# Kernel optimization log

Hardware: AMD Instinct MI355X
Metric: run time of the kernel (lower is better)

Reference implementation:

```python
import jax, jax.numpy as jnp
import numpy as np

C = 256          # C_in == C_out
G = C // 4       # groups = C_in/4 -> 4 channels per group
K = 3
STRIDE = 1
PAD = 2
DIL = 2
EPS = 1e-5

@jax.custom_vjp
def binarize(x):
    # 1-bit sign binarization with straight-through estimator (STE)
    return jnp.sign(x)

def _bin_fwd(x):
    return jnp.sign(x), x

def _bin_bwd(x, g):
    # STE with hardtanh clip: pass grad where |x| <= 1
    return (g * (jnp.abs(x) <= 1.0).astype(g.dtype),)

binarize.defvjp(_bin_fwd, _bin_bwd)

def setup_inputs() -> dict:
    key = jax.random.key(0)
    k1, k2, k3, k4, k5, k6 = jax.random.split(key, 6)
    x = jax.random.normal(k1, (64, C, 32, 32), jnp.float32)
    # grouped conv weight: [C_out, C_in/groups, K, K] = [256, 4, 3, 3]
    weight = jax.random.normal(k2, (C, C // G, K, K), jnp.float32) * 0.1
    gamma = 1.0 + 0.1 * jax.random.normal(k3, (C,), jnp.float32)
    beta = 0.1 * jax.random.normal(k4, (C,), jnp.float32)
    running_mean = 0.1 * jax.random.normal(k5, (C,), jnp.float32)
    running_var = jax.random.uniform(k6, (C,), jnp.float32, 0.5, 1.5)
    return {"x": x, "weight": weight, "gamma": gamma, "beta": beta,
            "running_mean": running_mean, "running_var": running_var}

def reference(x, weight, gamma, beta, running_mean, running_var):
    # BatchNorm2d (inference form with running stats)
    inv = gamma * jax.lax.rsqrt(running_var + EPS)            # [C]
    h = x * inv[None, :, None, None] + (beta - running_mean * inv)[None, :, None, None]
    # binarize activations and weights (1w1a)
    a = binarize(h)
    w = binarize(weight)
    # grouped dilated conv, stride 1, pad 2, dilation 2 -> same HxW
    out = jax.lax.conv_general_dilated(
        a, w,
        window_strides=(STRIDE, STRIDE),
        padding=[(PAD, PAD), (PAD, PAD)],
        rhs_dilation=(DIL, DIL),
        dimension_numbers=("NCHW", "OIHW", "NCHW"),
        feature_group_count=G)
    # channel shuffle: [N,C,H,W] -> [N,g,C/g,H,W] -> [N,C/g,g,H,W] -> [N,C,H,W]
    N, Cc, H, W = out.shape
    out = out.reshape(N, G, Cc // G, H, W).transpose(0, 2, 1, 3, 4).reshape(N, Cc, H, W)
    # identity shortcut (stride == 1)
    return out + x
```

## Files before the change

### kernel.cpp

```cpp
#include <hip/hip_runtime.h>

#ifndef __has_builtin
#define __has_builtin(x) 0
#endif

#if __has_builtin(__builtin_amdgcn_sdot4)
#define DOT4(a, b, c) __builtin_amdgcn_sdot4((a), (b), (c), false)
#else
__device__ __forceinline__ int dot4_sw(int a, int b, int c) {
#pragma unroll
    for (int k = 0; k < 4; ++k)
        c += (int)(signed char)((a >> (8 * k)) & 0xff) *
             (int)(signed char)((b >> (8 * k)) & 0xff);
    return c;
}
#define DOT4(a, b, c) dot4_sw((a), (b), (c))
#endif

#if __has_builtin(__builtin_amdgcn_sched_barrier)
#define SCHED_FENCE() __builtin_amdgcn_sched_barrier(0)
#else
#define SCHED_FENCE() asm volatile("" ::: "memory")
#endif

typedef float vfloat4 __attribute__((ext_vector_type(4)));

constexpr int CH   = 256;
constexpr int NPIX = 1024;
constexpr float BN_EPS = 1e-5f;

__global__ __launch_bounds__(64)
void bconv(const float* __restrict__ x,
           const float* __restrict__ wgt,
           const float* __restrict__ gamma,
           const float* __restrict__ beta,
           const float* __restrict__ rmean,
           const float* __restrict__ rvar,
           float* __restrict__ out) {
    const int lane = threadIdx.x;
    const int bid = blockIdx.x;
    const int swz = (bid & 7) * 2048 + (bid >> 3);
    const int oct = swz & 3;
    const int g   = (swz >> 2) & 63;
    const int n   = swz >> 8;

    const int row  = oct * 8 + (lane >> 3);
    const int col0 = (lane & 7) * 4;
    const int pix0 = row * 32 + col0;
    const float* xn = x + n * CH * NPIX;
    float* on = out + n * CH * NPIX;

    vfloat4 xv[3][4];
#pragma unroll
    for (int kh = 0; kh < 3; ++kh) {
        const int rsc = min(max(row + 2 * kh - 2, 0), 31);
        const float* rp = xn + g * 4 * NPIX + rsc * 32 + col0;
#pragma unroll
        for (int ci = 0; ci < 4; ++ci)
            xv[kh][ci] = *(const vfloat4*)(rp + ci * NPIX);
    }
    vfloat4 sc[4];
#pragma unroll
    for (int c2 = 0; c2 < 4; ++c2)
        sc[c2] = *(const vfloat4*)(xn + (c2 * 64 + g) * NPIX + pix0);
    SCHED_FENCE();

    const int* wb = (const int*)(wgt + g * 144);
    int wq[4][9];
#pragma unroll
    for (int c2 = 0; c2 < 4; ++c2)
#pragma unroll
        for (int t = 0; t < 9; ++t) {
            int pk = 0;
#pragma unroll
            for (int ci = 0; ci < 4; ++ci) {
                const int b = wb[c2 * 36 + ci * 9 + t];
                const int s = ((b & 0x7fffffff) == 0) ? 0 : ((b < 0) ? -1 : 1);
                pk |= (s & 0xff) << (8 * ci);
            }
            wq[c2][t] = pk;
        }

    float inv[4], bias[4];
#pragma unroll
    for (int ci = 0; ci < 4; ++ci) {
        const int c = g * 4 + ci;
        float r  = __fdiv_rn(1.0f, __fsqrt_rn(__fadd_rn(rvar[c], BN_EPS)));
        inv[ci]  = __fmul_rn(gamma[c], r);
        bias[ci] = __fsub_rn(beta[c], __fmul_rn(rmean[c], inv[ci]));
    }

    int pkc[3][4];
#pragma unroll
    for (int kh = 0; kh < 3; ++kh) {
        const bool ok = (unsigned)(row + 2 * kh - 2) < 32u;
#pragma unroll
        for (int p = 0; p < 4; ++p) {
            int v = 0;
#pragma unroll
            for (int ci = 0; ci < 4; ++ci) {
                float h = __fadd_rn(__fmul_rn(xv[kh][ci][p], inv[ci]), bias[ci]);
                int s = (h > 0.f) ? 1 : ((h < 0.f) ? -1 : 0);
                v |= (s & 0xff) << (8 * ci);
            }
            pkc[kh][p] = ok ? v : 0;
        }
    }

    const bool le = (col0 == 0), re = (col0 == 28);
    int a[3][8];
#pragma unroll
    for (int kh = 0; kh < 3; ++kh) {
        int l2 = __shfl_up(pkc[kh][2], 1);
        int l3 = __shfl_up(pkc[kh][3], 1);
        int r0 = __shfl_down(pkc[kh][0], 1);
        int r1 = __shfl_down(pkc[kh][1], 1);
        a[kh][0] = le ? 0 : l2;
        a[kh][1] = le ? 0 : l3;
        a[kh][2] = pkc[kh][0]; a[kh][3] = pkc[kh][1];
        a[kh][4] = pkc[kh][2]; a[kh][5] = pkc[kh][3];
        a[kh][6] = re ? 0 : r0;
        a[kh][7] = re ? 0 : r1;
    }

#pragma unroll
    for (int c2 = 0; c2 < 4; ++c2) {
        vfloat4 o;
#pragma unroll
        for (int p = 0; p < 4; ++p) {
            int acc = 0;
#pragma unroll
            for (int kh = 0; kh < 3; ++kh)
#pragma unroll
                for (int kw = 0; kw < 3; ++kw)
                    acc = DOT4(a[kh][p + 2 * kw], wq[c2][kh * 3 + kw], acc);
            o[p] = __fadd_rn((float)acc, sc[c2][p]);
        }
        __builtin_nontemporal_store(o, (vfloat4*)(on + (c2 * 64 + g) * NPIX + pix0));
    }
}

extern "C" void kernel_launch(void* const* d_in, const int* in_sizes, int n_in,
                              void* d_out, int out_size, void* d_ws, size_t ws_size,
                              hipStream_t stream) {
    const float* x     = (const float*)d_in[0];
    const float* wgt   = (const float*)d_in[1];
    const float* gamma = (const float*)d_in[2];
    const float* beta  = (const float*)d_in[3];
    const float* rmean = (const float*)d_in[4];
    const float* rvar  = (const float*)d_in[5];
    float* out = (float*)d_out;

    const int N = in_sizes[0] / (CH * NPIX);
    bconv<<<N * 64 * 4, 64, 0, stream>>>(x, wgt, gamma, beta, rmean, rvar, out);
}
```

Measured before the change: 35.53 us.

## Process eight images per block with double-buffered register prefetch

Each block now has 256 threads covering a whole 32x32 image for one group, and it loops over 8 images. It double-buffers the input loads in registers so the next image's loads overlap the current image's compute. Weight packing and BN constants are computed once per block instead of once per image tile. The trade-offs are higher register pressure (two buffers of 16+4 vfloat4), far fewer blocks (512 instead of 16384), and an assumption that N is a multiple of 8.

Result: faster. 31.82 us (-10.5%).

```diff
diff --git a/kernel.cpp b/kernel.cpp
--- a/kernel.cpp
+++ b/kernel.cpp
@@ -29,7 +29,7 @@
 constexpr int NPIX = 1024;
 constexpr float BN_EPS = 1e-5f;
 
-__global__ __launch_bounds__(64)
+__global__ __launch_bounds__(256, 2)
 void bconv(const float* __restrict__ x,
            const float* __restrict__ wgt,
            const float* __restrict__ gamma,
@@ -37,33 +37,15 @@
            const float* __restrict__ rmean,
            const float* __restrict__ rvar,
            float* __restrict__ out) {
-    const int lane = threadIdx.x;
+    const int tid = threadIdx.x;
     const int bid = blockIdx.x;
-    const int swz = (bid & 7) * 2048 + (bid >> 3);
-    const int oct = swz & 3;
-    const int g   = (swz >> 2) & 63;
-    const int n   = swz >> 8;
+    const int swz = (bid & 7) * 64 + (bid >> 3);
+    const int g   = swz & 63;
+    const int n0  = (swz >> 6) * 8;
 
-    const int row  = oct * 8 + (lane >> 3);
-    const int col0 = (lane & 7) * 4;
-    const int pix0 = row * 32 + col0;
-    const float* xn = x + n * CH * NPIX;
-    float* on = out + n * CH * NPIX;
-
-    vfloat4 xv[3][4];
-#pragma unroll
-    for (int kh = 0; kh < 3; ++kh) {
-        const int rsc = min(max(row + 2 * kh - 2, 0), 31);
-        const float* rp = xn + g * 4 * NPIX + rsc * 32 + col0;
-#pragma unroll
-        for (int ci = 0; ci < 4; ++ci)
-            xv[kh][ci] = *(const vfloat4*)(rp + ci * NPIX);
-    }
-    vfloat4 sc[4];
-#pragma unroll
-    for (int c2 = 0; c2 < 4; ++c2)
-        sc[c2] = *(const vfloat4*)(xn + (c2 * 64 + g) * NPIX + pix0);
-    SCHED_FENCE();
+    const int pix0 = tid * 4;
+    const int row  = pix0 >> 5;
+    const int col0 = pix0 & 31;
 
     const int* wb = (const int*)(wgt + g * 144);
     int wq[4][9];
@@ -90,53 +72,84 @@
         bias[ci] = __fsub_rn(beta[c], __fmul_rn(rmean[c], inv[ci]));
     }
 
-    int pkc[3][4];
+    auto load_img = [&](int n, vfloat4 xv[3][4], vfloat4 sc[4]) {
+        const float* xn = x + n * CH * NPIX;
 #pragma unroll
-    for (int kh = 0; kh < 3; ++kh) {
-        const bool ok = (unsigned)(row + 2 * kh - 2) < 32u;
+        for (int kh = 0; kh < 3; ++kh) {
+            const int rsc = min(max(row + 2 * kh - 2, 0), 31);
+            const float* rp = xn + g * 4 * NPIX + rsc * 32 + col0;
 #pragma unroll
-        for (int p = 0; p < 4; ++p) {
-            int v = 0;
+            for (int ci = 0; ci < 4; ++ci)
+                xv[kh][ci] = *(const vfloat4*)(rp + ci * NPIX);
+        }
 #pragma unroll
-            for (int ci = 0; ci < 4; ++ci) {
-                float h = __fadd_rn(__fmul_rn(xv[kh][ci][p], inv[ci]), bias[ci]);
-                int s = (h > 0.f) ? 1 : ((h < 0.f) ? -1 : 0);
-                v |= (s & 0xff) << (8 * ci);
-            }
-            pkc[kh][p] = ok ? v : 0;
-        }
-    }
+        for (int c2 = 0; c2 < 4; ++c2)
+            sc[c2] = *(const vfloat4*)(xn + (c2 * 64 + g) * NPIX + pix0);
+    };
 
     const bool le = (col0 == 0), re = (col0 == 28);
-    int a[3][8];
+    auto process = [&](int n, const vfloat4 xv[3][4], const vfloat4 sc[4]) {
+        int pkc[3][4];
 #pragma unroll
-    for (int kh = 0; kh < 3; ++kh) {
-        int l2 = __shfl_up(pkc[kh][2], 1);
-        int l3 = __shfl_up(pkc[kh][3], 1);
-        int r0 = __shfl_down(pkc[kh][0], 1);
-        int r1 = __shfl_down(pkc[kh][1], 1);
-        a[kh][0] = le ? 0 : l2;
-        a[kh][1] = le ? 0 : l3;
-        a[kh][2] = pkc[kh][0]; a[kh][3] = pkc[kh][1];
-        a[kh][4] = pkc[kh][2]; a[kh][5] = pkc[kh][3];
-        a[kh][6] = re ? 0 : r0;
-        a[kh][7] = re ? 0 : r1;
-    }
+        for (int kh = 0; kh < 3; ++kh) {
+            const bool ok = (unsigned)(row + 2 * kh - 2) < 32u;
+#pragma unroll
+            for (int p = 0; p < 4; ++p) {
+                int v = 0;
+#pragma unroll
+                for (int ci = 0; ci < 4; ++ci) {
+                    float h = __fadd_rn(__fmul_rn(xv[kh][ci][p], inv[ci]), bias[ci]);
+                    int s = (h > 0.f) ? 1 : ((h < 0.f) ? -1 : 0);
+                    v |= (s & 0xff) << (8 * ci);
+                }
+                pkc[kh][p] = ok ? v : 0;
+            }
+        }
+        int a[3][8];
+#pragma unroll
+        for (int kh = 0; kh < 3; ++kh) {
+            int l2 = __shfl_up(pkc[kh][2], 1);
+            int l3 = __shfl_up(pkc[kh][3], 1);
+            int r0 = __shfl_down(pkc[kh][0], 1);
+            int r1 = __shfl_down(pkc[kh][1], 1);
+            a[kh][0] = le ? 0 : l2;
+            a[kh][1] = le ? 0 : l3;
+            a[kh][2] = pkc[kh][0]; a[kh][3] = pkc[kh][1];
+            a[kh][4] = pkc[kh][2]; a[kh][5] = pkc[kh][3];
+            a[kh][6] = re ? 0 : r0;
+            a[kh][7] = re ? 0 : r1;
+        }
+        float* on = out + n * CH * NPIX;
+#pragma unroll
+        for (int c2 = 0; c2 < 4; ++c2) {
+            vfloat4 o;
+#pragma unroll
+            for (int p = 0; p < 4; ++p) {
+                int acc = 0;
+#pragma unroll
+                for (int kh = 0; kh < 3; ++kh)
+#pragma unroll
+                    for (int kw = 0; kw < 3; ++kw)
+                        acc = DOT4(a[kh][p + 2 * kw], wq[c2][kh * 3 + kw], acc);
+                o[p] = __fadd_rn((float)acc, sc[c2][p]);
+            }
+            __builtin_nontemporal_store(o, (vfloat4*)(on + (c2 * 64 + g) * NPIX + pix0));
+        }
+    };
 
+    vfloat4 xvA[3][4], scA[4], xvB[3][4], scB[4];
+    load_img(n0, xvA, scA);
 #pragma unroll
-    for (int c2 = 0; c2 < 4; ++c2) {
-        vfloat4 o;
-#pragma unroll
-        for (int p = 0; p < 4; ++p) {
-            int acc = 0;
-#pragma unroll
-            for (int kh = 0; kh < 3; ++kh)
-#pragma unroll
-                for (int kw = 0; kw < 3; ++kw)
-                    acc = DOT4(a[kh][p + 2 * kw], wq[c2][kh * 3 + kw], acc);
-            o[p] = __fadd_rn((float)acc, sc[c2][p]);
+    for (int ii = 0; ii < 4; ++ii) {
+        const int n = n0 + 2 * ii;
+        load_img(n + 1, xvB, scB);
+        SCHED_FENCE();
+        process(n, xvA, scA);
+        if (ii < 3) {
+            load_img(n + 2, xvA, scA);
+            SCHED_FENCE();
         }
-        __builtin_nontemporal_store(o, (vfloat4*)(on + (c2 * 64 + g) * NPIX + pix0));
+        process(n + 1, xvB, scB);
     }
 }
 
@@ -152,5 +165,5 @@
     float* out = (float*)d_out;
 
     const int N = in_sizes[0] / (CH * NPIX);
-    bconv<<<N * 64 * 4, 64, 0, stream>>>(x, wgt, gamma, beta, rmean, rvar, out);
+    bconv<<<(N / 8) * 64, 256, 0, stream>>>(x, wgt, gamma, beta, rmean, rvar, out);
 }
```
